# Performance work log

Measured on AMD Instinct MI355X. Metric: run time of the kernel, lower is better.

The kernel has to match this reference:

```python
import jax, jax.numpy as jnp
import numpy as np

B, T, C_IN, HID, WIN = 16384, 20, 256, 256, 3


def tb_mask(T=20, win=3):
    # Faithful replica of TemporalCrossAttent.TB (including its quirky indexing).
    m = np.zeros((T, T), dtype=np.float32)
    for i in range(T):
        if i - win < 0:
            m[i, :win] = 1
        elif i + win >= T:
            m[i, T - win:] = 1
        else:
            m[i - win // 2, i - win // 2:i + win // 2] = 1
    return jnp.asarray(np.where(m == 1, 0.0, -1e22).astype(np.float32))


def setup_inputs() -> dict:
    key = jax.random.key(0)
    k1, k2, k3, k4, k5 = jax.random.split(key, 5)
    scale = 0.05  # xavier-ish init scale for 256x256
    return {
        "feat1": jax.random.normal(k1, (B, T, C_IN), dtype=jnp.float32),
        "feat2": jax.random.normal(k2, (B, T, C_IN), dtype=jnp.float32),
        "Wq": jax.random.normal(k3, (HID, C_IN), dtype=jnp.float32) * scale,
        "Wk": jax.random.normal(k4, (HID, C_IN), dtype=jnp.float32) * scale,
        "Wv": jax.random.normal(k5, (HID, C_IN), dtype=jnp.float32) * scale,
    }


def reference(feat1, feat2, Wq, Wk, Wv):
    # Conv1d(kernel_size=1, bias=False) == pointwise linear over channels.
    mask = tb_mask(T, WIN)  # [T, T] static banded additive mask
    q = jnp.einsum('btc,hc->bth', feat1, Wq)  # [B,T,HID]
    k = jnp.einsum('btc,hc->bth', feat2, Wk)
    v = jnp.einsum('btc,hc->bth', feat2, Wv)
    sim = jnp.einsum('bth,bsh->bts', q, k) / jnp.sqrt(jnp.float32(HID))
    attn = jax.nn.softmax(sim + mask, axis=-1)  # [B,T,T]
    # dropout layers act as identity in eval mode
    return jnp.einsum('bts,bsh->bth', attn, v)  # [B,T,HID]
```

## Files before the change

kernel.cpp:

```cpp
#include <hip/hip_runtime.h>
#include <stdint.h>

#define NBATCH 16384
#define TT     20
#define CC     256
#define NB     2
#define RPAD   48
#define LDK    264

typedef __bf16 bf16x8 __attribute__((ext_vector_type(8)));
typedef float  f32x4  __attribute__((ext_vector_type(4)));

__constant__ int8_t c_CNT[TT]     = {3,3,4,2,2,2,2,2,2,2,2,2,2,2,2,2,0,3,3,3};
__constant__ int8_t c_OFF[TT]     = {0,3,6,10,12,14,16,18,20,22,24,26,28,30,32,34,0,36,39,42};
__constant__ int8_t c_COLS[TT][4] = {
    {0,1,2,0},{0,1,2,0},{0,1,2,3},
    {3,4,0,0},{4,5,0,0},{5,6,0,0},{6,7,0,0},{7,8,0,0},{8,9,0,0},
    {9,10,0,0},{10,11,0,0},{11,12,0,0},{12,13,0,0},{13,14,0,0},
    {14,15,0,0},{15,16,0,0},{0,0,0,0},
    {17,18,19,0},{17,18,19,0},{17,18,19,0}};
__constant__ int8_t c_PT[45] = {0,0,0,1,1,1,2,2,2,2,3,3,4,4,5,5,6,6,7,7,8,8,9,9,
                                10,10,11,11,12,12,13,13,14,14,15,15,17,17,17,18,18,18,19,19,19};
__constant__ int8_t c_PS[45] = {0,1,2,0,1,2,0,1,2,3,3,4,4,5,5,6,6,7,7,8,8,9,9,10,
                                10,11,11,12,12,13,13,14,14,15,15,16,17,18,19,17,18,19,17,18,19};

__device__ __forceinline__ uint32_t f2bf1(float f) {
    uint32_t u = __builtin_bit_cast(uint32_t, f);
    return (u + 0x7fffu + ((u >> 16) & 1u)) >> 16;
}
__device__ __forceinline__ uint32_t pack2(float a, float b) { return f2bf1(a) | (f2bf1(b) << 16); }
__device__ __forceinline__ float bflo(uint32_t u) { return __builtin_bit_cast(float, u << 16); }
__device__ __forceinline__ float bfhi(uint32_t u) { return __builtin_bit_cast(float, u & 0xffff0000u); }

__global__ void prep_kernel(const float* __restrict__ Wq, const float* __restrict__ Wk,
                            const float* __restrict__ Wv, uint16_t* __restrict__ mqkT,
                            uint16_t* __restrict__ wvb) {
    const int n = blockIdx.x;
    const int k = threadIdx.x;
    float acc = 0.f;
    for (int h = 0; h < CC; ++h)
        acc = fmaf(Wk[h * CC + n], Wq[h * CC + k], acc);
    mqkT[n * CC + k] = (uint16_t)f2bf1(acc * 0.0625f);
    wvb[n * CC + k]  = (uint16_t)f2bf1(Wv[n * CC + k]);
}

__device__ __forceinline__ void gemm48(const uint16_t* __restrict__ sA,
                                       const uint16_t* __restrict__ Bg,
                                       int lrow, int lk8, f32x4 acc[3][4]) {
#pragma unroll
    for (int kk = 0; kk < 8; ++kk) {
        bf16x8 av[3], bv[4];
#pragma unroll
        for (int rt = 0; rt < 3; ++rt) {
            uint4 u = *(const uint4*)(sA + (rt * 16 + lrow) * LDK + kk * 32 + lk8);
            av[rt] = __builtin_bit_cast(bf16x8, u);
        }
#pragma unroll
        for (int ct = 0; ct < 4; ++ct) {
            uint4 u = *(const uint4*)(Bg + (ct * 16 + lrow) * CC + kk * 32 + lk8);
            bv[ct] = __builtin_bit_cast(bf16x8, u);
        }
#pragma unroll
        for (int rt = 0; rt < 3; ++rt)
#pragma unroll
            for (int ct = 0; ct < 4; ++ct)
                acc[rt][ct] = __builtin_amdgcn_mfma_f32_16x16x32_bf16(av[rt], bv[ct], acc[rt][ct], 0, 0, 0);
    }
}

__device__ __forceinline__ void store48(uint16_t* __restrict__ sD, int w, int lane, f32x4 acc[3][4]) {
    const int drow = (lane >> 4) << 2;
    const int dcol = lane & 15;
#pragma unroll
    for (int rt = 0; rt < 3; ++rt)
#pragma unroll
        for (int ct = 0; ct < 4; ++ct)
#pragma unroll
            for (int i = 0; i < 4; ++i)
                sD[(rt * 16 + drow + i) * LDK + (w * 64 + ct * 16 + dcol)] =
                    (uint16_t)f2bf1(acc[rt][ct][i]);
}

__device__ __forceinline__ void acc8(float* o, uint4 uv, float wgt) {
    o[0] = fmaf(bflo(uv.x), wgt, o[0]);
    o[1] = fmaf(bfhi(uv.x), wgt, o[1]);
    o[2] = fmaf(bflo(uv.y), wgt, o[2]);
    o[3] = fmaf(bfhi(uv.y), wgt, o[3]);
    o[4] = fmaf(bflo(uv.z), wgt, o[4]);
    o[5] = fmaf(bfhi(uv.z), wgt, o[5]);
    o[6] = fmaf(bflo(uv.w), wgt, o[6]);
    o[7] = fmaf(bfhi(uv.w), wgt, o[7]);
}

__global__ __launch_bounds__(256, 3)
void attn_main(const float* __restrict__ f1g, const float* __restrict__ f2g,
               const uint16_t* __restrict__ mqkT, const uint16_t* __restrict__ wvb,
               float* __restrict__ outg) {
    __shared__ uint16_t sA2[RPAD * LDK];
    __shared__ uint16_t sA1[RPAD * LDK];
    __shared__ float s_sim[NB * 45];
    __shared__ float s_attn[NB * TT * 4];

    const int tid  = threadIdx.x;
    const int lane = tid & 63;
    const int w    = tid >> 6;
    const int lrow = lane & 15;
    const int lk8  = (lane >> 4) << 3;
    const int b0   = blockIdx.x * NB;

    const float* f1 = f1g + (size_t)b0 * TT * CC;
    const float* f2 = f2g + (size_t)b0 * TT * CC;

#pragma unroll
    for (int i = 0; i < 10; ++i) {
        int idx = tid + (i << 8);
        int r   = idx >> 6;
        int c4  = (idx & 63) << 2;
        float4 a = *(const float4*)(f1 + (idx << 2));
        float4 b = *(const float4*)(f2 + (idx << 2));
        uint2 ua; ua.x = pack2(a.x, a.y); ua.y = pack2(a.z, a.w);
        uint2 ub; ub.x = pack2(b.x, b.y); ub.y = pack2(b.z, b.w);
        *(uint2*)&sA1[r * LDK + c4] = ua;
        *(uint2*)&sA2[r * LDK + c4] = ub;
    }
    for (int i = tid; i < 8 * LDK; i += 256) {
        sA1[40 * LDK + i] = 0;
        sA2[40 * LDK + i] = 0;
    }
    __syncthreads();

    f32x4 acc[3][4];
#pragma unroll
    for (int a = 0; a < 3; ++a)
#pragma unroll
        for (int b = 0; b < 4; ++b)
            acc[a][b] = f32x4{0.f, 0.f, 0.f, 0.f};
    gemm48(sA1, mqkT + w * 64 * CC, lrow, lk8, acc);
    __syncthreads();
    store48(sA1, w, lane, acc);
    __syncthreads();

    if (tid < 180) {
        int d  = tid >> 1;
        int p  = tid & 1;
        int lb = (d >= 45) ? 1 : 0;
        int pd = d - lb * 45;
        int t = c_PT[pd], s = c_PS[pd];
        const uint16_t* ap = &sA1[(lb * 20 + t) * LDK + (p << 7)];
        const uint16_t* bp = &sA2[(lb * 20 + s) * LDK + (p << 7)];
        float da = 0.f;
#pragma unroll
        for (int c = 0; c < 128; c += 8) {
            uint4 ua = *(const uint4*)(ap + c);
            uint4 ub = *(const uint4*)(bp + c);
            da = fmaf(bflo(ua.x), bflo(ub.x), da);
            da = fmaf(bfhi(ua.x), bfhi(ub.x), da);
            da = fmaf(bflo(ua.y), bflo(ub.y), da);
            da = fmaf(bfhi(ua.y), bfhi(ub.y), da);
            da = fmaf(bflo(ua.z), bflo(ub.z), da);
            da = fmaf(bfhi(ua.z), bfhi(ub.z), da);
            da = fmaf(bflo(ua.w), bflo(ub.w), da);
            da = fmaf(bfhi(ua.w), bfhi(ub.w), da);
        }
        da += __shfl_xor(da, 1);
        if (p == 0) s_sim[d] = da;
    }
    __syncthreads();

#pragma unroll
    for (int a = 0; a < 3; ++a)
#pragma unroll
        for (int b = 0; b < 4; ++b)
            acc[a][b] = f32x4{0.f, 0.f, 0.f, 0.f};
    gemm48(sA2, wvb + w * 64 * CC, lrow, lk8, acc);

    if (tid < NB * TT) {
        int lb = (tid >= TT) ? 1 : 0;
        int t  = tid - lb * TT;
        int cnt = c_CNT[t];
        if (cnt) {
            int off = lb * 45 + c_OFF[t];
            float m = -1e30f;
#pragma unroll
            for (int j = 0; j < 4; ++j)
                if (j < cnt) m = fmaxf(m, s_sim[off + j]);
            float ee[4] = {0.f, 0.f, 0.f, 0.f};
            float ssum = 0.f;
#pragma unroll
            for (int j = 0; j < 4; ++j)
                if (j < cnt) { ee[j] = __expf(s_sim[off + j] - m); ssum += ee[j]; }
            float inv = 1.f / ssum;
#pragma unroll
            for (int j = 0; j < 4; ++j)
                if (j < cnt) s_attn[(lb * TT + t) * 4 + j] = ee[j] * inv;
        }
    }
    __syncthreads();
    store48(sA1, w, lane, acc);
    __syncthreads();

    const size_t outbase = (size_t)b0 * TT * CC;
#pragma unroll
    for (int i = 0; i < 5; ++i) {
        int u  = tid + (i << 8);
        int r  = u >> 5;
        int ch = (u & 31) << 3;
        int lb = (r >= TT) ? 1 : 0;
        int t  = r - lb * TT;
        float o[8] = {0.f, 0.f, 0.f, 0.f, 0.f, 0.f, 0.f, 0.f};
        if (t == 16) {
            const uint16_t* base = &sA1[(lb * TT) * LDK + ch];
#pragma unroll
            for (int s = 0; s < TT; ++s) {
                uint4 uv = *(const uint4*)(base + s * LDK);
                acc8(o, uv, 0.05f);
            }
        } else {
            int cnt = c_CNT[t];
#pragma unroll
            for (int j = 0; j < 4; ++j) {
                if (j < cnt) {
                    float wgt = s_attn[(lb * TT + t) * 4 + j];
                    int s = c_COLS[t][j];
                    uint4 uv = *(const uint4*)&sA1[(lb * TT + s) * LDK + ch];
                    acc8(o, uv, wgt);
                }
            }
        }
        float* op = outg + outbase + (size_t)r * CC + ch;
        *(float4*)op       = make_float4(o[0], o[1], o[2], o[3]);
        *(float4*)(op + 4) = make_float4(o[4], o[5], o[6], o[7]);
    }
}

extern "C" void kernel_launch(void* const* d_in, const int* in_sizes, int n_in,
                              void* d_out, int out_size, void* d_ws, size_t ws_size,
                              hipStream_t stream) {
    const float* feat1 = (const float*)d_in[0];
    const float* feat2 = (const float*)d_in[1];
    const float* Wq    = (const float*)d_in[2];
    const float* Wk    = (const float*)d_in[3];
    const float* Wv    = (const float*)d_in[4];
    uint16_t* mqkT = (uint16_t*)d_ws;
    uint16_t* wvb  = mqkT + CC * CC;

    prep_kernel<<<CC, CC, 0, stream>>>(Wq, Wk, Wv, mqkT, wvb);
    attn_main<<<NBATCH / NB, 256, 0, stream>>>(feat1, feat2, mqkT, wvb, (float*)d_out);
}
```

Measured before the change: 401.4 us.

## Process one batch per block, load feat1 directly into MFMA fragments, shrink LDS

Each block now handles one batch instead of two, reducing LDS to two 20-row tiles and raising the launch-bounds occupancy target from 3 to 6 blocks. feat1 is read straight from global memory and converted to bf16 in registers for the Q·Mqk GEMM, skipping the LDS staging pass and zero-padding. The GEMMs use two 16-row tiles (32 rows) instead of three, with row-guarded stores, and the dot-product stage splits work four ways per pair. The costs are that weight-matrix B loads are spread over twice as many blocks, and the direct global reads of feat1 use a less coalesced access pattern.

```diff
diff --git a/kernel.cpp b/kernel.cpp
--- a/kernel.cpp
+++ b/kernel.cpp
@@ -4,8 +4,6 @@
 #define NBATCH 16384
 #define TT     20
 #define CC     256
-#define NB     2
-#define RPAD   48
 #define LDK    264
 
 typedef __bf16 bf16x8 __attribute__((ext_vector_type(8)));
@@ -24,13 +22,22 @@
 __constant__ int8_t c_PS[45] = {0,1,2,0,1,2,0,1,2,3,3,4,4,5,5,6,6,7,7,8,8,9,9,10,
                                 10,11,11,12,12,13,13,14,14,15,15,16,17,18,19,17,18,19,17,18,19};
 
-__device__ __forceinline__ uint32_t f2bf1(float f) {
-    uint32_t u = __builtin_bit_cast(uint32_t, f);
-    return (u + 0x7fffu + ((u >> 16) & 1u)) >> 16;
-}
-__device__ __forceinline__ uint32_t pack2(float a, float b) { return f2bf1(a) | (f2bf1(b) << 16); }
+__device__ __forceinline__ uint16_t f2bf(float f) {
+    __bf16 b = (__bf16)f;
+    return __builtin_bit_cast(uint16_t, b);
+}
+__device__ __forceinline__ uint32_t pk2(float a, float b) {
+    return (uint32_t)f2bf(a) | ((uint32_t)f2bf(b) << 16);
+}
 __device__ __forceinline__ float bflo(uint32_t u) { return __builtin_bit_cast(float, u << 16); }
 __device__ __forceinline__ float bfhi(uint32_t u) { return __builtin_bit_cast(float, u & 0xffff0000u); }
+
+__device__ __forceinline__ bf16x8 cvt8(float4 x, float4 y) {
+    bf16x8 r;
+    r[0] = (__bf16)x.x; r[1] = (__bf16)x.y; r[2] = (__bf16)x.z; r[3] = (__bf16)x.w;
+    r[4] = (__bf16)y.x; r[5] = (__bf16)y.y; r[6] = (__bf16)y.z; r[7] = (__bf16)y.w;
+    return r;
+}
 
 __global__ void prep_kernel(const float* __restrict__ Wq, const float* __restrict__ Wk,
                             const float* __restrict__ Wv, uint16_t* __restrict__ mqkT,
@@ -40,45 +47,24 @@
     float acc = 0.f;
     for (int h = 0; h < CC; ++h)
         acc = fmaf(Wk[h * CC + n], Wq[h * CC + k], acc);
-    mqkT[n * CC + k] = (uint16_t)f2bf1(acc * 0.0625f);
-    wvb[n * CC + k]  = (uint16_t)f2bf1(Wv[n * CC + k]);
-}
-
-__device__ __forceinline__ void gemm48(const uint16_t* __restrict__ sA,
-                                       const uint16_t* __restrict__ Bg,
-                                       int lrow, int lk8, f32x4 acc[3][4]) {
-#pragma unroll
-    for (int kk = 0; kk < 8; ++kk) {
-        bf16x8 av[3], bv[4];
-#pragma unroll
-        for (int rt = 0; rt < 3; ++rt) {
-            uint4 u = *(const uint4*)(sA + (rt * 16 + lrow) * LDK + kk * 32 + lk8);
-            av[rt] = __builtin_bit_cast(bf16x8, u);
-        }
-#pragma unroll
-        for (int ct = 0; ct < 4; ++ct) {
-            uint4 u = *(const uint4*)(Bg + (ct * 16 + lrow) * CC + kk * 32 + lk8);
-            bv[ct] = __builtin_bit_cast(bf16x8, u);
-        }
-#pragma unroll
-        for (int rt = 0; rt < 3; ++rt)
-#pragma unroll
-            for (int ct = 0; ct < 4; ++ct)
-                acc[rt][ct] = __builtin_amdgcn_mfma_f32_16x16x32_bf16(av[rt], bv[ct], acc[rt][ct], 0, 0, 0);
-    }
-}
-
-__device__ __forceinline__ void store48(uint16_t* __restrict__ sD, int w, int lane, f32x4 acc[3][4]) {
+    mqkT[n * CC + k] = f2bf(acc * 0.0625f);
+    wvb[n * CC + k]  = f2bf(Wv[n * CC + k]);
+}
+
+__device__ __forceinline__ void storeD(uint16_t* __restrict__ sD, int w, int lane,
+                                       f32x4 acc[2][4]) {
     const int drow = (lane >> 4) << 2;
     const int dcol = lane & 15;
 #pragma unroll
-    for (int rt = 0; rt < 3; ++rt)
+    for (int rt = 0; rt < 2; ++rt)
 #pragma unroll
         for (int ct = 0; ct < 4; ++ct)
 #pragma unroll
-            for (int i = 0; i < 4; ++i)
-                sD[(rt * 16 + drow + i) * LDK + (w * 64 + ct * 16 + dcol)] =
-                    (uint16_t)f2bf1(acc[rt][ct][i]);
+            for (int i = 0; i < 4; ++i) {
+                int row = rt * 16 + drow + i;
+                if (row < TT)
+                    sD[row * LDK + (w * 64 + ct * 16 + dcol)] = f2bf(acc[rt][ct][i]);
+            }
 }
 
 __device__ __forceinline__ void acc8(float* o, uint4 uv, float wgt) {
@@ -92,65 +78,82 @@
     o[7] = fmaf(bfhi(uv.w), wgt, o[7]);
 }
 
-__global__ __launch_bounds__(256, 3)
+__global__ __launch_bounds__(256, 6)
 void attn_main(const float* __restrict__ f1g, const float* __restrict__ f2g,
                const uint16_t* __restrict__ mqkT, const uint16_t* __restrict__ wvb,
                float* __restrict__ outg) {
-    __shared__ uint16_t sA2[RPAD * LDK];
-    __shared__ uint16_t sA1[RPAD * LDK];
-    __shared__ float s_sim[NB * 45];
-    __shared__ float s_attn[NB * TT * 4];
+    __shared__ uint16_t smem[2 * TT * LDK];
+    __shared__ float s_sim[45];
+    __shared__ float s_attn[TT * 4];
+    uint16_t* sF2 = smem;
+    uint16_t* sT  = smem + TT * LDK;
 
     const int tid  = threadIdx.x;
     const int lane = tid & 63;
     const int w    = tid >> 6;
     const int lrow = lane & 15;
     const int lk8  = (lane >> 4) << 3;
-    const int b0   = blockIdx.x * NB;
+    const int b0   = blockIdx.x;
 
     const float* f1 = f1g + (size_t)b0 * TT * CC;
     const float* f2 = f2g + (size_t)b0 * TT * CC;
 
 #pragma unroll
-    for (int i = 0; i < 10; ++i) {
+    for (int i = 0; i < 5; ++i) {
         int idx = tid + (i << 8);
         int r   = idx >> 6;
         int c4  = (idx & 63) << 2;
-        float4 a = *(const float4*)(f1 + (idx << 2));
         float4 b = *(const float4*)(f2 + (idx << 2));
-        uint2 ua; ua.x = pack2(a.x, a.y); ua.y = pack2(a.z, a.w);
-        uint2 ub; ub.x = pack2(b.x, b.y); ub.y = pack2(b.z, b.w);
-        *(uint2*)&sA1[r * LDK + c4] = ua;
-        *(uint2*)&sA2[r * LDK + c4] = ub;
-    }
-    for (int i = tid; i < 8 * LDK; i += 256) {
-        sA1[40 * LDK + i] = 0;
-        sA2[40 * LDK + i] = 0;
-    }
-    __syncthreads();
-
-    f32x4 acc[3][4];
-#pragma unroll
-    for (int a = 0; a < 3; ++a)
+        uint2 ub; ub.x = pk2(b.x, b.y); ub.y = pk2(b.z, b.w);
+        *(uint2*)&sF2[r * LDK + c4] = ub;
+    }
+
+    f32x4 acc[2][4];
+#pragma unroll
+    for (int a = 0; a < 2; ++a)
 #pragma unroll
         for (int b = 0; b < 4; ++b)
             acc[a][b] = f32x4{0.f, 0.f, 0.f, 0.f};
-    gemm48(sA1, mqkT + w * 64 * CC, lrow, lk8, acc);
+    {
+        const float* a0p = f1 + (size_t)lrow * CC + lk8;
+        const int grow1  = min(16 + lrow, TT - 1);
+        const float* a1p = f1 + (size_t)grow1 * CC + lk8;
+        const uint16_t* Bg = mqkT + w * 64 * CC;
+#pragma unroll
+        for (int kk = 0; kk < 8; ++kk) {
+            bf16x8 av[2], bv[4];
+            {
+                float4 x = *(const float4*)(a0p + kk * 32);
+                float4 y = *(const float4*)(a0p + kk * 32 + 4);
+                av[0] = cvt8(x, y);
+                x = *(const float4*)(a1p + kk * 32);
+                y = *(const float4*)(a1p + kk * 32 + 4);
+                av[1] = cvt8(x, y);
+            }
+#pragma unroll
+            for (int ct = 0; ct < 4; ++ct) {
+                uint4 u = *(const uint4*)(Bg + (ct * 16 + lrow) * CC + kk * 32 + lk8);
+                bv[ct] = __builtin_bit_cast(bf16x8, u);
+            }
+#pragma unroll
+            for (int rt = 0; rt < 2; ++rt)
+#pragma unroll
+                for (int ct = 0; ct < 4; ++ct)
+                    acc[rt][ct] = __builtin_amdgcn_mfma_f32_16x16x32_bf16(av[rt], bv[ct], acc[rt][ct], 0, 0, 0);
+        }
+    }
+    storeD(sT, w, lane, acc);
     __syncthreads();
-    store48(sA1, w, lane, acc);
-    __syncthreads();
 
     if (tid < 180) {
-        int d  = tid >> 1;
-        int p  = tid & 1;
-        int lb = (d >= 45) ? 1 : 0;
-        int pd = d - lb * 45;
-        int t = c_PT[pd], s = c_PS[pd];
-        const uint16_t* ap = &sA1[(lb * 20 + t) * LDK + (p << 7)];
-        const uint16_t* bp = &sA2[(lb * 20 + s) * LDK + (p << 7)];
+        int d = tid >> 2;
+        int p = tid & 3;
+        int t = c_PT[d], s = c_PS[d];
+        const uint16_t* ap = &sT[t * LDK + (p << 6)];
+        const uint16_t* bp = &sF2[s * LDK + (p << 6)];
         float da = 0.f;
 #pragma unroll
-        for (int c = 0; c < 128; c += 8) {
+        for (int c = 0; c < 64; c += 8) {
             uint4 ua = *(const uint4*)(ap + c);
             uint4 ub = *(const uint4*)(bp + c);
             da = fmaf(bflo(ua.x), bflo(ub.x), da);
@@ -163,23 +166,16 @@
             da = fmaf(bfhi(ua.w), bfhi(ub.w), da);
         }
         da += __shfl_xor(da, 1);
+        da += __shfl_xor(da, 2);
         if (p == 0) s_sim[d] = da;
     }
     __syncthreads();
 
-#pragma unroll
-    for (int a = 0; a < 3; ++a)
-#pragma unroll
-        for (int b = 0; b < 4; ++b)
-            acc[a][b] = f32x4{0.f, 0.f, 0.f, 0.f};
-    gemm48(sA2, wvb + w * 64 * CC, lrow, lk8, acc);
-
-    if (tid < NB * TT) {
-        int lb = (tid >= TT) ? 1 : 0;
-        int t  = tid - lb * TT;
+    if (tid < TT) {
+        int t = tid;
         int cnt = c_CNT[t];
         if (cnt) {
-            int off = lb * 45 + c_OFF[t];
+            int off = c_OFF[t];
             float m = -1e30f;
 #pragma unroll
             for (int j = 0; j < 4; ++j)
@@ -192,44 +188,70 @@
             float inv = 1.f / ssum;
 #pragma unroll
             for (int j = 0; j < 4; ++j)
-                if (j < cnt) s_attn[(lb * TT + t) * 4 + j] = ee[j] * inv;
-        }
-    }
+                if (j < cnt) s_attn[t * 4 + j] = ee[j] * inv;
+        }
+    }
+#pragma unroll
+    for (int a = 0; a < 2; ++a)
+#pragma unroll
+        for (int b = 0; b < 4; ++b)
+            acc[a][b] = f32x4{0.f, 0.f, 0.f, 0.f};
+    {
+        const uint16_t* Bg = wvb + w * 64 * CC;
+#pragma unroll
+        for (int kk = 0; kk < 8; ++kk) {
+            bf16x8 av[2], bv[4];
+#pragma unroll
+            for (int rt = 0; rt < 2; ++rt) {
+                uint4 u = *(const uint4*)(sF2 + (rt * 16 + lrow) * LDK + kk * 32 + lk8);
+                av[rt] = __builtin_bit_cast(bf16x8, u);
+            }
+#pragma unroll
+            for (int ct = 0; ct < 4; ++ct) {
+                uint4 u = *(const uint4*)(Bg + (ct * 16 + lrow) * CC + kk * 32 + lk8);
+                bv[ct] = __builtin_bit_cast(bf16x8, u);
+            }
+#pragma unroll
+            for (int rt = 0; rt < 2; ++rt)
+#pragma unroll
+                for (int ct = 0; ct < 4; ++ct)
+                    acc[rt][ct] = __builtin_amdgcn_mfma_f32_16x16x32_bf16(av[rt], bv[ct], acc[rt][ct], 0, 0, 0);
+        }
+    }
+    storeD(sT, w, lane, acc);
     __syncthreads();
-    store48(sA1, w, lane, acc);
-    __syncthreads();
 
     const size_t outbase = (size_t)b0 * TT * CC;
 #pragma unroll
-    for (int i = 0; i < 5; ++i) {
-        int u  = tid + (i << 8);
-        int r  = u >> 5;
-        int ch = (u & 31) << 3;
-        int lb = (r >= TT) ? 1 : 0;
-        int t  = r - lb * TT;
-        float o[8] = {0.f, 0.f, 0.f, 0.f, 0.f, 0.f, 0.f, 0.f};
-        if (t == 16) {
-            const uint16_t* base = &sA1[(lb * TT) * LDK + ch];
-#pragma unroll
-            for (int s = 0; s < TT; ++s) {
-                uint4 uv = *(const uint4*)(base + s * LDK);
-                acc8(o, uv, 0.05f);
-            }
-        } else {
-            int cnt = c_CNT[t];
-#pragma unroll
-            for (int j = 0; j < 4; ++j) {
-                if (j < cnt) {
-                    float wgt = s_attn[(lb * TT + t) * 4 + j];
-                    int s = c_COLS[t][j];
-                    uint4 uv = *(const uint4*)&sA1[(lb * TT + s) * LDK + ch];
-                    acc8(o, uv, wgt);
+    for (int i = 0; i < 3; ++i) {
+        int u = tid + (i << 8);
+        if (u < 640) {
+            int r  = u >> 5;
+            int ch = (u & 31) << 3;
+            float o[8] = {0.f, 0.f, 0.f, 0.f, 0.f, 0.f, 0.f, 0.f};
+            if (r == 16) {
+                const uint16_t* base = &sT[ch];
+#pragma unroll
+                for (int s = 0; s < TT; ++s) {
+                    uint4 uv = *(const uint4*)(base + s * LDK);
+                    acc8(o, uv, 0.05f);
                 }
-            }
-        }
-        float* op = outg + outbase + (size_t)r * CC + ch;
-        *(float4*)op       = make_float4(o[0], o[1], o[2], o[3]);
-        *(float4*)(op + 4) = make_float4(o[4], o[5], o[6], o[7]);
+            } else {
+                int cnt = c_CNT[r];
+#pragma unroll
+                for (int j = 0; j < 4; ++j) {
+                    if (j < cnt) {
+                        float wgt = s_attn[r * 4 + j];
+                        int s = c_COLS[r][j];
+                        uint4 uv = *(const uint4*)&sT[s * LDK + ch];
+                        acc8(o, uv, wgt);
+                    }
+                }
+            }
+            float* op = outg + outbase + (size_t)r * CC + ch;
+            *(float4*)op       = make_float4(o[0], o[1], o[2], o[3]);
+            *(float4*)(op + 4) = make_float4(o[4], o[5], o[6], o[7]);
+        }
     }
 }
 
@@ -245,5 +267,5 @@
     uint16_t* wvb  = mqkT + CC * CC;
 
     prep_kernel<<<CC, CC, 0, stream>>>(Wq, Wk, Wv, mqkT, wvb);
-    attn_main<<<NBATCH / NB, 256, 0, stream>>>(feat1, feat2, mqkT, wvb, (float*)d_out);
-}
+    attn_main<<<NBATCH, 256, 0, stream>>>(feat1, feat2, mqkT, wvb, (float*)d_out);
+}
```

Measured after the change: 798.0 us. +98.8%, slower.
